# Kernel tuning notes

Measured on AMD Instinct MI355X. Metric: run time of the kernel, lower is better.

The kernel has to match this reference:

```python
import jax, jax.numpy as jnp
import numpy as np

ALPHA = 0.2  # LeakyReLU negative slope


def gat_layer(x, W, a, alpha=ALPHA):
    """Multi-head dense GAT layer.
    x: (B, N, F); W: (H, F, O); a: (H, 2*O, 1).
    Returns (B, N, H*O) — ELU(head outputs) concatenated over heads.
    """
    H, F, O = W.shape
    Wh = jnp.einsum('bnf,hfo->bhno', x, W)          # (B,H,N,O)
    a_src = a[:, :O, 0]                              # (H,O)
    a_dst = a[:, O:, 0]                              # (H,O)
    s_src = jnp.einsum('bhno,ho->bhn', Wh, a_src)    # (B,H,N)
    s_dst = jnp.einsum('bhno,ho->bhn', Wh, a_dst)    # (B,H,N)
    e = s_src[..., :, None] + s_dst[..., None, :]    # (B,H,N,N)
    e = jax.nn.leaky_relu(e, negative_slope=alpha)
    att = jax.nn.softmax(e, axis=-1)                 # softmax over neighbors j
    out = jnp.einsum('bhnm,bhmo->bhno', att, Wh)     # (B,H,N,O)
    out = jax.nn.elu(out)
    B, _, N, _ = out.shape
    return jnp.transpose(out, (0, 2, 1, 3)).reshape(B, N, H * O)


def setup_inputs() -> dict:
    key = jax.random.key(0)
    ks = jax.random.split(key, 5)
    B, N = 32, 1024
    x = jax.random.normal(ks[0], (B, N, 4), dtype=jnp.float32)
    # layer1: nfeat=4, nhid=2, nheads=3
    W1 = jax.random.normal(ks[1], (3, 4, 2), dtype=jnp.float32) * 0.5
    a1 = jax.random.normal(ks[2], (3, 4, 1), dtype=jnp.float32) * 0.5
    # layer2: nfeat=6, nhid=4, nheads=1
    W2 = jax.random.normal(ks[3], (1, 6, 4), dtype=jnp.float32) * 0.5
    a2 = jax.random.normal(ks[4], (1, 8, 1), dtype=jnp.float32) * 0.5
    return {"x": x, "W1": W1, "a1": a1, "W2": W2, "a2": a2}


def reference(x, W1, a1, W2, a2):
    h = gat_layer(x, W1, a1)   # (B, N, 6)
    y = gat_layer(h, W2, a2)   # (B, N, 4)
    return y
```

## Files before the change

kernel.cpp:

```cpp
#include <hip/hip_runtime.h>


#define GAT_ALPHA 0.2f
#define LOG2E 1.44269504088896f

template <int F, int O, int H>
__global__ __launch_bounds__(256) void gat_layer_kernel(
    const float* __restrict__ x,
    const float* __restrict__ Wt,
    const float* __restrict__ at,
    float* __restrict__ out)
{
    constexpr int N = 1024, NT = 256, RPB = 128, S = 16, R = 8;
    constexpr int CHUNKS = N / RPB;
    constexpr int Q = O + 1;

    const int bid   = blockIdx.x;
    const int chunk = bid % CHUNKS;
    const int h     = (bid / CHUNKS) % H;
    const int b     = bid / (CHUNKS * H);
    const int tid   = threadIdx.x;
    const int r     = tid & 15;
    const int s     = tid >> 4;

    float Wl[F][O];
#pragma unroll
    for (int f = 0; f < F; ++f)
#pragma unroll
        for (int o = 0; o < O; ++o)
            Wl[f][o] = Wt[(h * F + f) * O + o];

    float asrc[O], adst[O];
#pragma unroll
    for (int o = 0; o < O; ++o) {
        asrc[o] = at[h * 2 * O + o];
        adst[o] = at[h * 2 * O + O + o];
    }

    __shared__ __align__(16) float sWh[N * O];
    __shared__ float2 sE[N];
    __shared__ float  sdp[N];
    __shared__ float  sred[4];
    __shared__ float  sredu[RPB * Q * S];
    __shared__ float  ssum[RPB * Q];

    const float* xb = x + (size_t)b * N * F;
    float dmax = -3.0e38f;
    for (int m = tid; m < N; m += NT) {
        float xv[F];
        if constexpr (F == 4) {
            const float4 v = ((const float4*)xb)[m];
            xv[0] = v.x; xv[1] = v.y; xv[2] = v.z; xv[3] = v.w;
        } else {
#pragma unroll
            for (int k = 0; k < F / 2; ++k) {
                const float2 v = ((const float2*)xb)[m * (F / 2) + k];
                xv[2 * k] = v.x; xv[2 * k + 1] = v.y;
            }
        }
        float d = 0.0f;
#pragma unroll
        for (int o = 0; o < O; ++o) {
            float wh = 0.0f;
#pragma unroll
            for (int f = 0; f < F; ++f) wh += xv[f] * Wl[f][o];
            sWh[m * O + o] = wh;
            d += wh * adst[o];
        }
        sdp[m] = d;
        dmax = fmaxf(dmax, d);
    }
#pragma unroll
    for (int off = 32; off > 0; off >>= 1)
        dmax = fmaxf(dmax, __shfl_xor(dmax, off, 64));
    if ((tid & 63) == 0) sred[tid >> 6] = dmax;
    __syncthreads();
    const float D = fmaxf(fmaxf(sred[0], sred[1]), fmaxf(sred[2], sred[3]));

    for (int m = tid; m < N; m += NT) {
        const float t = (sdp[m] - D) * LOG2E;
        sE[m] = make_float2(__builtin_amdgcn_exp2f(t),
                            __builtin_amdgcn_exp2f(GAT_ALPHA * t));
    }

    float thr[R], c1[R], c2[R];
#pragma unroll
    for (int j = 0; j < R; ++j) {
        const int row = chunk * RPB + r + 16 * j;
        float sn = 0.0f;
#pragma unroll
        for (int o = 0; o < O; ++o) sn += sWh[row * O + o] * asrc[o];
        const float z = sn + D;
        const float e = __builtin_amdgcn_exp2f(-0.8f * LOG2E * fabsf(z));
        c1[j] = (z >= 0.0f) ? 1.0f : e;
        c2[j] = (z >= 0.0f) ? e : 1.0f;
        thr[j] = -sn;
    }
    __syncthreads();

    float den[R], num[R][O];
#pragma unroll
    for (int j = 0; j < R; ++j) {
        den[j] = 0.0f;
#pragma unroll
        for (int o = 0; o < O; ++o) num[j][o] = 0.0f;
    }

#pragma unroll 4
    for (int mi = 0; mi < N / S; ++mi) {
        const int m = mi * S + s;
        const float  dm = sdp[m];
        const float2 E  = sE[m];
        float wp[O];
        if constexpr (O == 2) {
            const float2 wv = ((const float2*)sWh)[m];
            wp[0] = wv.x; wp[1] = wv.y;
        } else {
            const float4 wv = ((const float4*)sWh)[m];
            wp[0] = wv.x; wp[1] = wv.y; wp[2] = wv.z; wp[3] = wv.w;
        }
#pragma unroll
        for (int j = 0; j < R; ++j) {
            const float w = (dm >= thr[j]) ? (c1[j] * E.x) : (c2[j] * E.y);
            den[j] += w;
#pragma unroll
            for (int o = 0; o < O; ++o) num[j][o] += w * wp[o];
        }
    }

#pragma unroll
    for (int j = 0; j < R; ++j) {
        const int rowl = r + 16 * j;
        sredu[(rowl * Q + 0) * S + s] = den[j];
#pragma unroll
        for (int o = 0; o < O; ++o)
            sredu[(rowl * Q + 1 + o) * S + s] = num[j][o];
    }
    __syncthreads();

    for (int idx = tid; idx < RPB * Q; idx += NT) {
        float acc = 0.0f;
#pragma unroll
        for (int ss = 0; ss < S; ++ss) acc += sredu[idx * S + ss];
        ssum[idx] = acc;
    }
    __syncthreads();

    for (int idx = tid; idx < RPB * O; idx += NT) {
        const int rowl = idx / O, o = idx % O;
        const float inv = 1.0f / ssum[rowl * Q];
        float v = ssum[rowl * Q + 1 + o] * inv;
        v = (v > 0.0f) ? v : (__expf(v) - 1.0f);
        const int row = chunk * RPB + rowl;
        out[((size_t)b * N + row) * (H * O) + h * O + o] = v;
    }
}

extern "C" void kernel_launch(void* const* d_in, const int* in_sizes, int n_in,
                              void* d_out, int out_size, void* d_ws, size_t ws_size,
                              hipStream_t stream) {
    const float* x  = (const float*)d_in[0];
    const float* W1 = (const float*)d_in[1];
    const float* a1 = (const float*)d_in[2];
    const float* W2 = (const float*)d_in[3];
    const float* a2 = (const float*)d_in[4];

    float* h1 = (float*)d_ws;
    float* y  = (float*)d_out;

    constexpr int B = 32;
    gat_layer_kernel<4, 2, 3><<<B * 3 * 8, 256, 0, stream>>>(x, W1, a1, h1);
    gat_layer_kernel<6, 4, 1><<<B * 1 * 8, 256, 0, stream>>>(h1, W2, a2, y);
}
```

Before: 93.14 us.

## Pack score/exp/Wh into float4 LDS, use fmax weights, shuffle-reduce partials, halve rows per block

Stores d, both exponentials and the first two Wh components in one float4 per node, so the inner loop does one LDS load instead of several. The leaky-relu branch select is replaced by fmaxf of the two scaled exponentials. The partial sums are reduced across 4 lanes with shuffles, with only 4 wave slices going through LDS. Rows per block drop from 128 to 64, doubling the grid to improve occupancy, at the cost of recomputing Wh for every node in twice as many blocks.

```diff
diff --git a/kernel.cpp b/kernel.cpp
--- a/kernel.cpp
+++ b/kernel.cpp
@@ -4,45 +4,46 @@
 #define GAT_ALPHA 0.2f
 #define LOG2E 1.44269504088896f
 
-template <int F, int O, int H>
+template <int F, int O, int H, int RPB>
 __global__ __launch_bounds__(256) void gat_layer_kernel(
     const float* __restrict__ x,
     const float* __restrict__ Wt,
     const float* __restrict__ at,
     float* __restrict__ out)
 {
-    constexpr int N = 1024, NT = 256, RPB = 128, S = 16, R = 8;
+    constexpr int N = 1024, NT = 256, S = 16;
+    constexpr int R = RPB / 16;
+    constexpr int Q = O + 1;
     constexpr int CHUNKS = N / RPB;
-    constexpr int Q = O + 1;
+    constexpr int PAD = R * Q + 1;
 
     const int bid   = blockIdx.x;
     const int chunk = bid % CHUNKS;
     const int h     = (bid / CHUNKS) % H;
     const int b     = bid / (CHUNKS * H);
     const int tid   = threadIdx.x;
-    const int r     = tid & 15;
-    const int s     = tid >> 4;
+    const int wv    = tid >> 6;
+    const int l     = tid & 63;
+    const int r     = (l >> 2) & 15;
+    const int sq    = l & 3;
+    const int s     = (wv << 2) | sq;
 
-    float Wl[F][O];
+    float Wl[F][4];
 #pragma unroll
     for (int f = 0; f < F; ++f)
 #pragma unroll
-        for (int o = 0; o < O; ++o)
-            Wl[f][o] = Wt[(h * F + f) * O + o];
-
-    float asrc[O], adst[O];
+        for (int o = 0; o < O; ++o) Wl[f][o] = Wt[(h * F + f) * O + o];
+    float asrc[4], adst[4];
 #pragma unroll
     for (int o = 0; o < O; ++o) {
         asrc[o] = at[h * 2 * O + o];
         adst[o] = at[h * 2 * O + O + o];
     }
 
-    __shared__ __align__(16) float sWh[N * O];
-    __shared__ float2 sE[N];
-    __shared__ float  sdp[N];
+    __shared__ float4 sEW[N];
+    __shared__ float2 sW2[(O > 2) ? N : 1];
     __shared__ float  sred[4];
-    __shared__ float  sredu[RPB * Q * S];
-    __shared__ float  ssum[RPB * Q];
+    __shared__ float  sredu[4 * 16 * PAD];
 
     const float* xb = x + (size_t)b * N * F;
     float dmax = -3.0e38f;
@@ -58,98 +59,106 @@
                 xv[2 * k] = v.x; xv[2 * k + 1] = v.y;
             }
         }
-        float d = 0.0f;
+        float wh[4], d = 0.0f;
 #pragma unroll
         for (int o = 0; o < O; ++o) {
-            float wh = 0.0f;
+            float acc = 0.0f;
 #pragma unroll
-            for (int f = 0; f < F; ++f) wh += xv[f] * Wl[f][o];
-            sWh[m * O + o] = wh;
-            d += wh * adst[o];
+            for (int f = 0; f < F; ++f) acc += xv[f] * Wl[f][o];
+            wh[o] = acc; d += acc * adst[o];
         }
-        sdp[m] = d;
+        sEW[m] = make_float4(d, 0.0f, wh[0], wh[1]);
+        if constexpr (O > 2) sW2[m] = make_float2(wh[2], wh[3]);
         dmax = fmaxf(dmax, d);
     }
 #pragma unroll
-    for (int off = 32; off > 0; off >>= 1)
-        dmax = fmaxf(dmax, __shfl_xor(dmax, off, 64));
-    if ((tid & 63) == 0) sred[tid >> 6] = dmax;
+    for (int off = 32; off; off >>= 1) dmax = fmaxf(dmax, __shfl_xor(dmax, off, 64));
+    if (l == 0) sred[wv] = dmax;
     __syncthreads();
     const float D = fmaxf(fmaxf(sred[0], sred[1]), fmaxf(sred[2], sred[3]));
 
-    for (int m = tid; m < N; m += NT) {
-        const float t = (sdp[m] - D) * LOG2E;
-        sE[m] = make_float2(__builtin_amdgcn_exp2f(t),
-                            __builtin_amdgcn_exp2f(GAT_ALPHA * t));
-    }
-
-    float thr[R], c1[R], c2[R];
+    float c1[R], c2[R];
 #pragma unroll
     for (int j = 0; j < R; ++j) {
         const int row = chunk * RPB + r + 16 * j;
-        float sn = 0.0f;
-#pragma unroll
-        for (int o = 0; o < O; ++o) sn += sWh[row * O + o] * asrc[o];
+        const float4 ew = sEW[row];
+        float sn = ew.z * asrc[0] + ew.w * asrc[1];
+        if constexpr (O > 2) {
+            const float2 w2 = sW2[row];
+            sn += w2.x * asrc[2] + w2.y * asrc[3];
+        }
         const float z = sn + D;
         const float e = __builtin_amdgcn_exp2f(-0.8f * LOG2E * fabsf(z));
         c1[j] = (z >= 0.0f) ? 1.0f : e;
         c2[j] = (z >= 0.0f) ? e : 1.0f;
-        thr[j] = -sn;
+    }
+
+    for (int m = tid; m < N; m += NT) {
+        const float t = (sEW[m].x - D) * LOG2E;
+        sEW[m].x = __builtin_amdgcn_exp2f(t);
+        sEW[m].y = __builtin_amdgcn_exp2f(GAT_ALPHA * t);
     }
     __syncthreads();
 
-    float den[R], num[R][O];
+    float den[R], num[R][4];
 #pragma unroll
     for (int j = 0; j < R; ++j) {
         den[j] = 0.0f;
 #pragma unroll
-        for (int o = 0; o < O; ++o) num[j][o] = 0.0f;
+        for (int o = 0; o < 4; ++o) num[j][o] = 0.0f;
     }
 
 #pragma unroll 4
     for (int mi = 0; mi < N / S; ++mi) {
         const int m = mi * S + s;
-        const float  dm = sdp[m];
-        const float2 E  = sE[m];
-        float wp[O];
-        if constexpr (O == 2) {
-            const float2 wv = ((const float2*)sWh)[m];
-            wp[0] = wv.x; wp[1] = wv.y;
-        } else {
-            const float4 wv = ((const float4*)sWh)[m];
-            wp[0] = wv.x; wp[1] = wv.y; wp[2] = wv.z; wp[3] = wv.w;
-        }
+        const float4 ew = sEW[m];
+        float w2x = 0.0f, w2y = 0.0f;
+        if constexpr (O > 2) { const float2 t2 = sW2[m]; w2x = t2.x; w2y = t2.y; }
 #pragma unroll
         for (int j = 0; j < R; ++j) {
-            const float w = (dm >= thr[j]) ? (c1[j] * E.x) : (c2[j] * E.y);
-            den[j] += w;
-#pragma unroll
-            for (int o = 0; o < O; ++o) num[j][o] += w * wp[o];
+            const float wgt = fmaxf(c1[j] * ew.x, c2[j] * ew.y);
+            den[j]    += wgt;
+            num[j][0] += wgt * ew.z;
+            num[j][1] += wgt * ew.w;
+            if constexpr (O > 2) {
+                num[j][2] += wgt * w2x;
+                num[j][3] += wgt * w2y;
+            }
         }
     }
 
 #pragma unroll
     for (int j = 0; j < R; ++j) {
-        const int rowl = r + 16 * j;
-        sredu[(rowl * Q + 0) * S + s] = den[j];
+        den[j] += __shfl_xor(den[j], 1, 64);
+        den[j] += __shfl_xor(den[j], 2, 64);
 #pragma unroll
-        for (int o = 0; o < O; ++o)
-            sredu[(rowl * Q + 1 + o) * S + s] = num[j][o];
+        for (int o = 0; o < O; ++o) {
+            num[j][o] += __shfl_xor(num[j][o], 1, 64);
+            num[j][o] += __shfl_xor(num[j][o], 2, 64);
+        }
     }
-    __syncthreads();
-
-    for (int idx = tid; idx < RPB * Q; idx += NT) {
-        float acc = 0.0f;
+    if (sq == 0) {
 #pragma unroll
-        for (int ss = 0; ss < S; ++ss) acc += sredu[idx * S + ss];
-        ssum[idx] = acc;
+        for (int j = 0; j < R; ++j) {
+            const int base = (wv * 16 + r) * PAD + j * Q;
+            sredu[base] = den[j];
+#pragma unroll
+            for (int o = 0; o < O; ++o) sredu[base + 1 + o] = num[j][o];
+        }
     }
     __syncthreads();
 
     for (int idx = tid; idx < RPB * O; idx += NT) {
         const int rowl = idx / O, o = idx % O;
-        const float inv = 1.0f / ssum[rowl * Q];
-        float v = ssum[rowl * Q + 1 + o] * inv;
+        const int rr = rowl & 15, jj = rowl >> 4;
+        float dn = 0.0f, nm = 0.0f;
+#pragma unroll
+        for (int ww = 0; ww < 4; ++ww) {
+            const int base = (ww * 16 + rr) * PAD + jj * Q;
+            dn += sredu[base];
+            nm += sredu[base + 1 + o];
+        }
+        float v = nm / dn;
         v = (v > 0.0f) ? v : (__expf(v) - 1.0f);
         const int row = chunk * RPB + rowl;
         out[((size_t)b * N + row) * (H * O) + h * O + o] = v;
@@ -169,6 +178,6 @@
     float* y  = (float*)d_out;
 
     constexpr int B = 32;
-    gat_layer_kernel<4, 2, 3><<<B * 3 * 8, 256, 0, stream>>>(x, W1, a1, h1);
-    gat_layer_kernel<6, 4, 1><<<B * 1 * 8, 256, 0, stream>>>(h1, W2, a2, y);
+    gat_layer_kernel<4, 2, 3, 64><<<B * 3 * 16, 256, 0, stream>>>(x, W1, a1, h1);
+    gat_layer_kernel<6, 4, 1, 64><<<B * 1 * 16, 256, 0, stream>>>(h1, W2, a2, y);
 }
```

After: 94.66 us. No clear change (+1.6%).
